# Performance work log

Measured on AMD Instinct MI355X. Metric: run time of the kernel, lower is better.

## Reference

```python
import jax, jax.numpy as jnp
import numpy as np

N_MOTIF_PER_CLASS = 8
N_CLASS = 16
N_MOTIF = N_MOTIF_PER_CLASS * N_CLASS
TEMPERATURE = 0.2
TAU = 0.99
K2 = 32
EPS = 1e-4


def setup_inputs() -> dict:
    key = jax.random.key(0)
    k1, k2, k3 = jax.random.split(key, 3)
    N, H = 32768, 1024
    z = jax.random.normal(k1, (N, H), dtype=jnp.float32)
    Motif_Vector = jax.random.normal(k2, (N_MOTIF, H), dtype=jnp.float32)
    y = jax.random.randint(k3, (N,), 0, N_CLASS, dtype=jnp.int64)
    return {"z": z, "Motif_Vector": Motif_Vector, "y": y}


def euclidean_1(X, M):
    # squared euclidean distance via GEMM, then log-ratio similarity
    xp = X @ M.T                                     # [N, n_motif]
    distance = (-2.0 * xp
                + jnp.sum(X * X, axis=1, keepdims=True)
                + jnp.sum(M * M, axis=1)[None, :])
    similarity = jnp.log((distance + 1.0) / (distance + EPS))
    return similarity, distance


def reference(z, Motif_Vector, y):
    similarity, distance = euclidean_1(z, Motif_Vector)

    # mapping: motif j belongs to class j // n_motif_per_class
    motif_class = jnp.arange(N_MOTIF) // N_MOTIF_PER_CLASS   # [n_motif]
    true_motifs = (y[:, None] == motif_class[None, :])       # [N, n_motif]

    # contrastive loss (exact torch math: exp(sim/T), max over positives,
    # sum over negatives)
    sims = jnp.exp(similarity / TEMPERATURE)
    sim_pos = jnp.max(jnp.where(true_motifs, sims, -jnp.inf), axis=1)
    sim_neg_sum = jnp.sum(jnp.where(true_motifs, 0.0, sims), axis=1)
    loss = -jnp.mean(jnp.log(sim_pos / (sim_neg_sum + sim_pos)))

    # update_motif (update_type='topk', weighted_mean=False):
    # torch passes `distance` into filter_similar_graph and argsorts
    # descending, i.e. selects the K2 LARGEST distances among same-class
    # samples (faithful to source).
    masked = jnp.where(true_motifs.T, distance.T, -jnp.inf)  # [n_motif, N]
    _, idx = jax.lax.top_k(masked, K2)                       # [n_motif, K2]
    selected = z[idx]                                        # [n_motif, K2, H]
    new_motif = jnp.mean(selected, axis=1)                   # weights = 1/K2
    new_M = TAU * Motif_Vector + (1.0 - TAU) * new_motif

    return loss, new_M
```

## Files before the change

### kernel.cpp

```cpp
#include <hip/hip_runtime.h>
#include <cstdint>
#include <cmath>

#define NROWS 32768
#define HD    1024
#define NMOT  128
#define NCLS  16
#define KSEL  32
#define EPSV  1e-4f

typedef __attribute__((ext_vector_type(4))) float  f32x4;
typedef __attribute__((ext_vector_type(8))) __bf16 bf16x8;
typedef __attribute__((ext_vector_type(4))) __bf16 bf16x4;
typedef unsigned long long u64;

#define WS_MN   64
#define WS_MVBF 256
#define WS_CD   65792
#define WS_S1K  327936

static __device__ __forceinline__ float dot4(float4 v) {
    return v.x * v.x + v.y * v.y + v.z * v.z + v.w * v.w;
}

static __device__ __forceinline__ bf16x4 cvt4(float4 v) {
    bf16x4 t;
    t[0] = (__bf16)v.x; t[1] = (__bf16)v.y; t[2] = (__bf16)v.z; t[3] = (__bf16)v.w;
    return t;
}

static __device__ __forceinline__ u64 pack_key(float v, int idx) {
    unsigned int b = __float_as_uint(v);
    unsigned int mo = (b & 0x80000000u) ? ~b : (b | 0x80000000u);
    unsigned int khi = ~mo;
    return ((u64)khi << 32) | (unsigned int)idx;
}

__global__ __launch_bounds__(256) void prep_k(const float* __restrict__ mv,
                                              float* __restrict__ wsf,
                                              __bf16* __restrict__ mvbf) {
    const int j = blockIdx.x;
    const int k = threadIdx.x * 4;
    float4 v = *(const float4*)&mv[(size_t)j * HD + k];
    *(bf16x4*)&mvbf[(size_t)j * HD + k] = cvt4(v);
    float s = dot4(v);
#pragma unroll
    for (int o = 1; o < 64; o <<= 1) s += __shfl_xor(s, o, 64);
    __shared__ float red[4];
    if ((threadIdx.x & 63) == 0) red[threadIdx.x >> 6] = s;
    __syncthreads();
    if (threadIdx.x == 0) {
        wsf[WS_MN + j] = red[0] + red[1] + red[2] + red[3];
        if (j == 0) wsf[0] = 0.f;
    }
}

#define BM 64
#define BN 128
#define BK 32
#define SA 40

__global__ __launch_bounds__(256, 2) void gemm_fused(
    const float* __restrict__ z, const __bf16* __restrict__ mvbf,
    const float* __restrict__ mn, float* __restrict__ cd,
    const int* __restrict__ y, float* __restrict__ lossAcc) {
    __shared__ __bf16 As[2][BM * SA];
    __shared__ __bf16 Bs[2][BN * SA];
    __shared__ float  szn[BM];
    __shared__ int    ly[BM];
    __shared__ float  spm[2][BM];
    __shared__ float  sns[2][BM];

    const int tid  = threadIdx.x;
    const int row0 = blockIdx.x * BM;
    const int lane = tid & 63;
    const int wave = tid >> 6;
    const int wr   = wave >> 1;
    const int wc   = wave & 1;
    const int l15  = lane & 15;
    const int quad = lane >> 4;

    const int sq = tid & 7;
    const int sr = tid >> 3;
    const int bq = tid & 3;
    const int br = tid >> 2;

    if (tid < BM) ly[tid] = y[row0 + tid];

    f32x4 acc[2][4];
#pragma unroll
    for (int i = 0; i < 2; ++i)
#pragma unroll
        for (int j = 0; j < 4; ++j) acc[i][j] = (f32x4){0.f, 0.f, 0.f, 0.f};

    float zsq0 = 0.f, zsq1 = 0.f;

    const float*  zb = z + (size_t)(row0 + sr) * HD + sq * 4;
    const __bf16* bb = mvbf + (size_t)br * HD + bq * 8;

    float4 a0 = *(const float4*)(zb);
    float4 a1 = *(const float4*)(zb + 32 * HD);
    bf16x8 b0 = *(const bf16x8*)(bb);
    bf16x8 b1 = *(const bf16x8*)(bb + 64 * HD);
    *(bf16x4*)&As[0][sr * SA + sq * 4]        = cvt4(a0);
    *(bf16x4*)&As[0][(sr + 32) * SA + sq * 4] = cvt4(a1);
    *(bf16x8*)&Bs[0][br * SA + bq * 8]        = b0;
    *(bf16x8*)&Bs[0][(br + 64) * SA + bq * 8] = b1;
    zsq0 += dot4(a0); zsq1 += dot4(a1);
    a0 = *(const float4*)(zb + BK);
    a1 = *(const float4*)(zb + BK + 32 * HD);
    b0 = *(const bf16x8*)(bb + BK);
    b1 = *(const bf16x8*)(bb + BK + 64 * HD);

    for (int kt = 0; kt < HD / BK; ++kt) {
        __syncthreads();
        if (kt + 1 < HD / BK) {
            const int w = (kt + 1) & 1;
            *(bf16x4*)&As[w][sr * SA + sq * 4]        = cvt4(a0);
            *(bf16x4*)&As[w][(sr + 32) * SA + sq * 4] = cvt4(a1);
            *(bf16x8*)&Bs[w][br * SA + bq * 8]        = b0;
            *(bf16x8*)&Bs[w][(br + 64) * SA + bq * 8] = b1;
            zsq0 += dot4(a0); zsq1 += dot4(a1);
            if (kt + 2 < HD / BK) {
                const float*  zn = zb + (kt + 2) * BK;
                const __bf16* bn = bb + (kt + 2) * BK;
                a0 = *(const float4*)(zn);
                a1 = *(const float4*)(zn + 32 * HD);
                b0 = *(const bf16x8*)(bn);
                b1 = *(const bf16x8*)(bn + 64 * HD);
            }
        }
        const int rb = kt & 1;
        const int ko = quad * 8;
        bf16x8 af[2], bfr[4];
#pragma unroll
        for (int i = 0; i < 2; ++i)
            af[i] = *(const bf16x8*)&As[rb][(wr * 32 + i * 16 + l15) * SA + ko];
#pragma unroll
        for (int j = 0; j < 4; ++j)
            bfr[j] = *(const bf16x8*)&Bs[rb][(wc * 64 + j * 16 + l15) * SA + ko];
#pragma unroll
        for (int i = 0; i < 2; ++i)
#pragma unroll
            for (int j = 0; j < 4; ++j)
                acc[i][j] = __builtin_amdgcn_mfma_f32_16x16x32_bf16(
                    af[i], bfr[j], acc[i][j], 0, 0, 0);
    }

#pragma unroll
    for (int o = 1; o < 8; o <<= 1) {
        zsq0 += __shfl_xor(zsq0, o, 64);
        zsq1 += __shfl_xor(zsq1, o, 64);
    }
    if (sq == 0) { szn[sr] = zsq0; szn[sr + 32] = zsq1; }
    __syncthreads();

    f32x4 znv[2];
    int rcls[2][4];
#pragma unroll
    for (int i = 0; i < 2; ++i) {
        znv[i] = *(const f32x4*)&szn[wr * 32 + i * 16 + quad * 4];
#pragma unroll
        for (int reg = 0; reg < 4; ++reg)
            rcls[i][reg] = ly[wr * 32 + i * 16 + quad * 4 + reg];
    }
    float pm[2][4], ns[2][4];
#pragma unroll
    for (int i = 0; i < 2; ++i)
#pragma unroll
        for (int reg = 0; reg < 4; ++reg) { pm[i][reg] = 0.f; ns[i][reg] = 0.f; }

#pragma unroll
    for (int j = 0; j < 4; ++j) {
        const int c = wc * 64 + j * 16 + l15;
        const float mc = mn[c];
        const int ccls = c >> 3;
#pragma unroll
        for (int i = 0; i < 2; ++i) {
#pragma unroll
            for (int reg = 0; reg < 4; ++reg) {
                const int row = wr * 32 + i * 16 + quad * 4 + reg;
                float d = znv[i][reg] + mc - 2.f * acc[i][j][reg];
                float r = (d + 1.0f) * __builtin_amdgcn_rcpf(d + EPSV);
                float r2 = r * r;
                float s = r2 * r2 * r;
                if (ccls == rcls[i][reg]) {
                    pm[i][reg] = fmaxf(pm[i][reg], s);
                    cd[(size_t)(row0 + row) * 8 + (c & 7)] = d;
                } else {
                    ns[i][reg] += s;
                }
            }
        }
    }
#pragma unroll
    for (int o = 1; o < 16; o <<= 1) {
#pragma unroll
        for (int i = 0; i < 2; ++i)
#pragma unroll
            for (int reg = 0; reg < 4; ++reg) {
                pm[i][reg] = fmaxf(pm[i][reg], __shfl_xor(pm[i][reg], o, 64));
                ns[i][reg] += __shfl_xor(ns[i][reg], o, 64);
            }
    }
    if (l15 == 0) {
#pragma unroll
        for (int i = 0; i < 2; ++i)
#pragma unroll
            for (int reg = 0; reg < 4; ++reg) {
                const int row = wr * 32 + i * 16 + quad * 4 + reg;
                spm[wc][row] = pm[i][reg];
                sns[wc][row] = ns[i][reg];
            }
    }
    __syncthreads();
    if (tid < BM) {
        float p = fmaxf(spm[0][tid], spm[1][tid]);
        float nsum = sns[0][tid] + sns[1][tid];
        float li = logf((nsum + p) / p);
#pragma unroll
        for (int o = 1; o < 64; o <<= 1) li += __shfl_xor(li, o, 64);
        if (tid == 0) atomicAdd(lossAcc, li);
    }
}

__global__ __launch_bounds__(256) void sel1_k(const int* __restrict__ y,
                                              const float* __restrict__ cd,
                                              u64* __restrict__ s1k) {
    __shared__ u64 keys[512];
    __shared__ int cnt;

    const int bid = blockIdx.x;
    const int j = bid >> 3, chunk = bid & 7;
    const int cls = j >> 3, m8 = j & 7;
    const int tid = threadIdx.x;
    const int lane = tid & 63;
    if (tid == 0) cnt = 0;
    __syncthreads();

    const int base = chunk * 4096;
#pragma unroll
    for (int t = 0; t < 16; ++t) {
        const int i = base + t * 256 + tid;
        const bool pred = (y[i] == cls);
        const u64 m = __ballot(pred);
        int wbase = 0;
        if (lane == 0 && m) wbase = atomicAdd(&cnt, (int)__popcll(m));
        wbase = __shfl(wbase, 0, 64);
        if (pred) {
            const int p = wbase + (int)__popcll(m & ((1ull << lane) - 1ull));
            if (p < 512) keys[p] = pack_key(cd[(size_t)i * 8 + m8], i);
        }
    }
    __syncthreads();
    const int n = cnt < 512 ? cnt : 512;
    for (int t = tid; t < 512; t += 256)
        if (t >= n) keys[t] = ~0ull;
    __syncthreads();

    for (int k = 2; k <= 512; k <<= 1) {
        for (int jj = k >> 1; jj > 0; jj >>= 1) {
            const int i  = ((tid & ~(jj - 1)) << 1) | (tid & (jj - 1));
            const int ix = i | jj;
            const u64 A = keys[i], B = keys[ix];
            const bool up = ((i & k) == 0);
            if ((A > B) == up) { keys[i] = B; keys[ix] = A; }
            __syncthreads();
        }
    }
    if (tid < KSEL) s1k[(size_t)bid * KSEL + tid] = keys[tid];
}

__global__ __launch_bounds__(256) void merge_k(
    const float* __restrict__ z, const float* __restrict__ mv,
    const u64* __restrict__ s1k, const float* __restrict__ lossAcc,
    float* __restrict__ out) {
    __shared__ u64 keys[256];
    __shared__ int sel[KSEL];

    const int b = blockIdx.x;
    const int j = b >> 2, q = b & 3;
    const int tid = threadIdx.x;
    keys[tid] = s1k[(size_t)j * 256 + tid];
    __syncthreads();

    for (int k = 2; k <= 256; k <<= 1) {
        for (int jj = k >> 1; jj > 0; jj >>= 1) {
            if (tid < 128) {
                const int i  = ((tid & ~(jj - 1)) << 1) | (tid & (jj - 1));
                const int ix = i | jj;
                const u64 A = keys[i], B = keys[ix];
                const bool up = ((i & k) == 0);
                if ((A > B) == up) { keys[i] = B; keys[ix] = A; }
            }
            __syncthreads();
        }
    }
    if (tid < KSEL) sel[tid] = (int)(keys[tid] & 0xFFFFFFFFu);
    __syncthreads();

    const int h = q * 256 + tid;
    float s = 0.f;
#pragma unroll 8
    for (int r = 0; r < KSEL; ++r) s += z[(size_t)sel[r] * HD + h];
    out[1 + (size_t)j * HD + h] =
        0.99f * mv[(size_t)j * HD + h] + 0.01f * (s * (1.0f / KSEL));
    if (b == 0 && tid == 0) out[0] = lossAcc[0] * (1.0f / NROWS);
}

extern "C" void kernel_launch(void* const* d_in, const int* in_sizes, int n_in,
                              void* d_out, int out_size, void* d_ws, size_t ws_size,
                              hipStream_t stream) {
    const float* z  = (const float*)d_in[0];
    const float* mv = (const float*)d_in[1];
    const int*   y  = (const int*)d_in[2];
    float* out = (float*)d_out;
    float* wsf = (float*)d_ws;
    float*  mn   = wsf + WS_MN;
    __bf16* mvbf = (__bf16*)(wsf + WS_MVBF);
    float*  cd   = wsf + WS_CD;
    u64*    s1k  = (u64*)(wsf + WS_S1K);

    hipLaunchKernelGGL(prep_k,     dim3(NMOT),       dim3(256), 0, stream, mv, wsf, mvbf);
    hipLaunchKernelGGL(gemm_fused, dim3(NROWS / BM), dim3(256), 0, stream, z, mvbf, mn, cd, y, wsf);
    hipLaunchKernelGGL(sel1_k,     dim3(NMOT * 8),   dim3(256), 0, stream, y, cd, s1k);
    hipLaunchKernelGGL(merge_k,    dim3(NMOT * 4),   dim3(256), 0, stream, z, mv, s1k, wsf, out);
}
```

Before: 239.8 us.

## Deepen GEMM global-load prefetch to four stages with register ring buffer

Replaces the single-stage register prefetch in the fused GEMM with a four-deep register ring, so global loads of z and motif tiles are issued four K-steps ahead. The inner loop is unrolled by four and LDS writes for the next tile are placed after the fragment reads and before the MFMAs, with one barrier per step. This is meant to hide HBM latency on the memory-bound z stream, at the cost of more VGPRs, which may pressure occupancy under launch_bounds(256,2).

```diff
diff --git a/kernel.cpp b/kernel.cpp
--- a/kernel.cpp
+++ b/kernel.cpp
@@ -58,6 +58,7 @@
 #define BM 64
 #define BN 128
 #define BK 32
+#define NS (HD / BK)
 #define SA 40
 
 __global__ __launch_bounds__(256, 2) void gemm_fused(
@@ -98,53 +99,64 @@
     const float*  zb = z + (size_t)(row0 + sr) * HD + sq * 4;
     const __bf16* bb = mvbf + (size_t)br * HD + bq * 8;
 
-    float4 a0 = *(const float4*)(zb);
-    float4 a1 = *(const float4*)(zb + 32 * HD);
-    bf16x8 b0 = *(const bf16x8*)(bb);
-    bf16x8 b1 = *(const bf16x8*)(bb + 64 * HD);
-    *(bf16x4*)&As[0][sr * SA + sq * 4]        = cvt4(a0);
-    *(bf16x4*)&As[0][(sr + 32) * SA + sq * 4] = cvt4(a1);
-    *(bf16x8*)&Bs[0][br * SA + bq * 8]        = b0;
-    *(bf16x8*)&Bs[0][(br + 64) * SA + bq * 8] = b1;
-    zsq0 += dot4(a0); zsq1 += dot4(a1);
-    a0 = *(const float4*)(zb + BK);
-    a1 = *(const float4*)(zb + BK + 32 * HD);
-    b0 = *(const bf16x8*)(bb + BK);
-    b1 = *(const bf16x8*)(bb + BK + 64 * HD);
-
-    for (int kt = 0; kt < HD / BK; ++kt) {
-        __syncthreads();
-        if (kt + 1 < HD / BK) {
-            const int w = (kt + 1) & 1;
-            *(bf16x4*)&As[w][sr * SA + sq * 4]        = cvt4(a0);
-            *(bf16x4*)&As[w][(sr + 32) * SA + sq * 4] = cvt4(a1);
-            *(bf16x8*)&Bs[w][br * SA + bq * 8]        = b0;
-            *(bf16x8*)&Bs[w][(br + 64) * SA + bq * 8] = b1;
-            zsq0 += dot4(a0); zsq1 += dot4(a1);
-            if (kt + 2 < HD / BK) {
-                const float*  zn = zb + (kt + 2) * BK;
-                const __bf16* bn = bb + (kt + 2) * BK;
-                a0 = *(const float4*)(zn);
-                a1 = *(const float4*)(zn + 32 * HD);
-                b0 = *(const bf16x8*)(bn);
-                b1 = *(const bf16x8*)(bn + 64 * HD);
-            }
-        }
-        const int rb = kt & 1;
-        const int ko = quad * 8;
-        bf16x8 af[2], bfr[4];
-#pragma unroll
-        for (int i = 0; i < 2; ++i)
-            af[i] = *(const bf16x8*)&As[rb][(wr * 32 + i * 16 + l15) * SA + ko];
-#pragma unroll
-        for (int j = 0; j < 4; ++j)
-            bfr[j] = *(const bf16x8*)&Bs[rb][(wc * 64 + j * 16 + l15) * SA + ko];
-#pragma unroll
-        for (int i = 0; i < 2; ++i)
+    float4 ra0[4], ra1[4];
+    bf16x8 rb0[4], rb1[4];
+#pragma unroll
+    for (int s = 0; s < 4; ++s) {
+        ra0[s] = *(const float4*)(zb + s * BK);
+        ra1[s] = *(const float4*)(zb + s * BK + 32 * HD);
+        rb0[s] = *(const bf16x8*)(bb + s * BK);
+        rb1[s] = *(const bf16x8*)(bb + s * BK + 64 * HD);
+    }
+    *(bf16x4*)&As[0][sr * SA + sq * 4]        = cvt4(ra0[0]);
+    *(bf16x4*)&As[0][(sr + 32) * SA + sq * 4] = cvt4(ra1[0]);
+    *(bf16x8*)&Bs[0][br * SA + bq * 8]        = rb0[0];
+    *(bf16x8*)&Bs[0][(br + 64) * SA + bq * 8] = rb1[0];
+    zsq0 += dot4(ra0[0]); zsq1 += dot4(ra1[0]);
+    ra0[0] = *(const float4*)(zb + 4 * BK);
+    ra1[0] = *(const float4*)(zb + 4 * BK + 32 * HD);
+    rb0[0] = *(const bf16x8*)(bb + 4 * BK);
+    rb1[0] = *(const bf16x8*)(bb + 4 * BK + 64 * HD);
+    __syncthreads();
+
+    for (int it = 0; it < NS / 4; ++it) {
+#pragma unroll
+        for (int u = 0; u < 4; ++u) {
+            const int kt = it * 4 + u;
+            const int rbuf = kt & 1;
+            const int ko = quad * 8;
+            bf16x8 af[2], bfr[4];
+#pragma unroll
+            for (int i = 0; i < 2; ++i)
+                af[i] = *(const bf16x8*)&As[rbuf][(wr * 32 + i * 16 + l15) * SA + ko];
 #pragma unroll
             for (int j = 0; j < 4; ++j)
-                acc[i][j] = __builtin_amdgcn_mfma_f32_16x16x32_bf16(
-                    af[i], bfr[j], acc[i][j], 0, 0, 0);
+                bfr[j] = *(const bf16x8*)&Bs[rbuf][(wc * 64 + j * 16 + l15) * SA + ko];
+            if (kt + 1 < NS) {
+                const int w = (kt + 1) & 1;
+                const int s = (kt + 1) & 3;
+                *(bf16x4*)&As[w][sr * SA + sq * 4]        = cvt4(ra0[s]);
+                *(bf16x4*)&As[w][(sr + 32) * SA + sq * 4] = cvt4(ra1[s]);
+                *(bf16x8*)&Bs[w][br * SA + bq * 8]        = rb0[s];
+                *(bf16x8*)&Bs[w][(br + 64) * SA + bq * 8] = rb1[s];
+                zsq0 += dot4(ra0[s]); zsq1 += dot4(ra1[s]);
+                if (kt + 5 < NS) {
+                    const float*  zn = zb + (kt + 5) * BK;
+                    const __bf16* bn = bb + (kt + 5) * BK;
+                    ra0[s] = *(const float4*)(zn);
+                    ra1[s] = *(const float4*)(zn + 32 * HD);
+                    rb0[s] = *(const bf16x8*)(bn);
+                    rb1[s] = *(const bf16x8*)(bn + 64 * HD);
+                }
+            }
+#pragma unroll
+            for (int i = 0; i < 2; ++i)
+#pragma unroll
+                for (int j = 0; j < 4; ++j)
+                    acc[i][j] = __builtin_amdgcn_mfma_f32_16x16x32_bf16(
+                        af[i], bfr[j], acc[i][j], 0, 0, 0);
+            __syncthreads();
+        }
     }
 
 #pragma unroll
```

New measurement: 236.7 us. No clear change (-1.3%).
